# Optimization experiments

Hardware: AMD Instinct MI355X
Metric: run time of the kernel (lower is better)

## Reference

```python
import jax, jax.numpy as jnp
import numpy as np

# Static multi-scale feature pyramid shapes (value_shapes arg of MSDeformAttn.forward)
VALUE_SHAPES = ((80, 80), (40, 40), (20, 20), (10, 10))
N_HEADS, N_LEVELS, N_POINTS, D_MODEL = 8, 4, 4, 256


def setup_inputs() -> dict:
    key = jax.random.key(0)
    ks = jax.random.split(key, 11)
    bs, lq, d = 16, 1000, D_MODEL
    lv = sum(h * w for h, w in VALUE_SHAPES)  # 8500
    s = 0.02  # weight scale
    f32 = jnp.float32
    return {
        "query": jax.random.normal(ks[0], (bs, lq, d), f32),
        "refer_bbox": jax.random.uniform(ks[1], (bs, lq, 1, 4), f32),  # cxcywh in [0,1]
        "value": jax.random.normal(ks[2], (bs, lv, d), f32),
        "W_off": jax.random.normal(ks[3], (d, N_HEADS * N_LEVELS * N_POINTS * 2), f32) * s,
        "b_off": jax.random.normal(ks[4], (N_HEADS * N_LEVELS * N_POINTS * 2,), f32) * s,
        "W_attn": jax.random.normal(ks[5], (d, N_HEADS * N_LEVELS * N_POINTS), f32) * s,
        "b_attn": jax.random.normal(ks[6], (N_HEADS * N_LEVELS * N_POINTS,), f32) * s,
        "W_val": jax.random.normal(ks[7], (d, d), f32) * s,
        "b_val": jax.random.normal(ks[8], (d,), f32) * s,
        "W_out": jax.random.normal(ks[9], (d, d), f32) * s,
        "b_out": jax.random.normal(ks[10], (d,), f32) * s,
    }


def _bilinear_sample(v, x, y):
    """grid_sample(mode=bilinear, padding=zeros, align_corners=False) equivalent.
    v: [bs, H, W, nh, dh]; x, y: pixel-space coords [bs, lq, nh, P].
    Returns [bs, lq, nh, P, dh]."""
    bs, H, W, nh, dh = v.shape
    x0f = jnp.floor(x)
    y0f = jnp.floor(y)
    wx = x - x0f  # fractional weights
    wy = y - y0f
    x0 = x0f.astype(jnp.int32)
    y0 = y0f.astype(jnp.int32)
    x1, y1 = x0 + 1, y0 + 1
    b_idx = jnp.arange(bs)[:, None, None, None]
    h_idx = jnp.arange(nh)[None, None, :, None]

    def gather(yi, xi):
        valid = (xi >= 0) & (xi < W) & (yi >= 0) & (yi < H)
        xc = jnp.clip(xi, 0, W - 1)
        yc = jnp.clip(yi, 0, H - 1)
        val = v[b_idx, yc, xc, h_idx]  # [bs, lq, nh, P, dh]
        return val * valid[..., None].astype(v.dtype)

    return (gather(y0, x0) * ((1 - wx) * (1 - wy))[..., None]
            + gather(y0, x1) * (wx * (1 - wy))[..., None]
            + gather(y1, x0) * ((1 - wx) * wy)[..., None]
            + gather(y1, x1) * (wx * wy)[..., None])


def reference(query, refer_bbox, value, W_off, b_off, W_attn, b_attn, W_val, b_val, W_out, b_out):
    bs, lq, d = query.shape
    nh, L, P = N_HEADS, N_LEVELS, N_POINTS
    dh = d // nh

    # value projection
    v = value @ W_val + b_val  # [bs, lv, d]
    v = v.reshape(bs, -1, nh, dh)

    # sampling offsets and attention weights from query
    offsets = (query @ W_off + b_off).reshape(bs, lq, nh, L, P, 2)
    attn = (query @ W_attn + b_attn).reshape(bs, lq, nh, L * P)
    attn = jax.nn.softmax(attn, axis=-1).reshape(bs, lq, nh, L, P)

    # refer_bbox: [bs, lq, 1, 4] cxcywh; num_points == 4 branch
    add = offsets / P * refer_bbox[:, :, None, :, None, 2:] * 0.5
    loc = refer_bbox[:, :, None, :, None, :2] + add  # [bs, lq, nh, L, P, 2] in [0,1]

    out = jnp.zeros((bs, lq, nh, dh), query.dtype)
    start = 0
    for l, (H, W) in enumerate(VALUE_SHAPES):
        vl = v[:, start:start + H * W].reshape(bs, H, W, nh, dh)
        start += H * W
        ll = loc[:, :, :, l]  # [bs, lq, nh, P, 2]
        # normalized [0,1] -> pixel coords (align_corners=False): p = loc*size - 0.5
        x = ll[..., 0] * W - 0.5
        y = ll[..., 1] * H - 0.5
        sampled = _bilinear_sample(vl, x, y)  # [bs, lq, nh, P, dh]
        out = out + jnp.einsum('bqhpd,bqhp->bqhd', sampled, attn[:, :, :, l])

    out = out.reshape(bs, lq, d)
    return out @ W_out + b_out
```

## Files before the change

### kernel.cpp

```cpp
#include <hip/hip_runtime.h>
#include <cstdint>
#include <cstddef>


typedef unsigned short u16;
typedef u16 u16x8 __attribute__((ext_vector_type(8)));
typedef __bf16 bf16x8 __attribute__((ext_vector_type(8)));
typedef float f32x4 __attribute__((ext_vector_type(4)));

__device__ inline u16 f2bf(float f) {
  return __builtin_bit_cast(u16, (__bf16)f);
}

__device__ __forceinline__ void glds16(const void* g, void* l) {
  __builtin_amdgcn_global_load_lds(
      (const __attribute__((address_space(1))) void*)g,
      (__attribute__((address_space(3))) void*)l, 16, 0, 0);
}

__global__ __launch_bounds__(256) void wconv(
    const float* __restrict__ W0, const float* __restrict__ W1,
    const float* __restrict__ W2, const float* __restrict__ W3,
    u16* __restrict__ T0, u16* __restrict__ T1, u16* __restrict__ T2,
    u16* __restrict__ T3) {
  __shared__ u16 tile[64][65];
  const float* Ws[4] = {W0, W1, W2, W3};
  u16* Ts[4] = {T0, T1, T2, T3};
  const int Ns[4] = {256, 256, 128, 256};
  const int z = blockIdx.z;
  const int N = Ns[z];
  const int n0 = blockIdx.x * 64;
  if (n0 >= N) return;
  const int k0 = blockIdx.y * 64;
  const float* W = Ws[z];
  u16* Wt = Ts[z];
  const int tr = threadIdx.x >> 6;
  const int tc = threadIdx.x & 63;
#pragma unroll
  for (int r = 0; r < 64; r += 4)
    tile[r + tr][tc] = f2bf(W[(size_t)(k0 + r + tr) * N + n0 + tc]);
  __syncthreads();
#pragma unroll
  for (int r = 0; r < 64; r += 4)
    Wt[(size_t)(n0 + r + tr) * 256 + k0 + tc] = tile[tc][r + tr];
}

template <int WAVES, int NF, bool OUT_BF16>
__global__ __launch_bounds__(WAVES * 64, 1) void gemm_p2(
    const float* __restrict__ A, const u16* __restrict__ Wt,
    const float* __restrict__ bias, void* __restrict__ Cv,
    int M, int NT, int G) {
  constexpr int N = NF * 16;
  constexpr int TR = WAVES * 16;
  constexpr int STN = OUT_BF16 ? (NF / 2) : NF;
  __shared__ __align__(16) u16 Bls[N * 256];
  __shared__ __align__(16) float Asub[WAVES * 1024];
  const int wave = threadIdx.x >> 6;
  const int lane = threadIdx.x & 63;
  const int lr = lane & 15;
  const int lj = lane >> 4;

  constexpr int NI = NF * 8 / WAVES;
#pragma unroll
  for (int g = 0; g < NI; ++g) {
    int inst = wave * NI + g;
    int s2 = inst * 2 + (lane >> 5);
    int pc = lane & 31;
    int jc = pc ^ (s2 & 7);
    int c = (s2 & 15) * NF + (s2 >> 4);
    glds16((const char*)Wt + (size_t)c * 512 + (size_t)jc * 16,
           (char*)Bls + inst * 1024);
  }

  float bv[NF];
#pragma unroll
  for (int ni = 0; ni < NF; ++ni) bv[ni] = bias[lr * NF + ni];

  char* aw = (char*)Asub + wave * 4096;

  auto stageA = [&](int t, int s, int buf) {
#pragma unroll
    for (int i = 0; i < 2; ++i) {
      long row = (long)t * TR + wave * 16 + i * 8 + (lane >> 3);
      if (row > (long)M - 1) row = M - 1;
      int jc = (lane & 7) ^ (lane >> 3);
      glds16((const char*)A + row * 1024 + (size_t)s * 128 + (size_t)jc * 16,
             aw + buf * 2048 + i * 1024);
    }
  };

  stageA(blockIdx.x, 0, 0);
  stageA(blockIdx.x, 1, 1);
  __syncthreads();

  for (int t = blockIdx.x; t < NT; t += G) {
    f32x4 acc[NF] = {};
#pragma unroll
    for (int s = 0; s < 8; ++s) {
      if (s < 2) {
        if constexpr (STN == 8)
          asm volatile("s_waitcnt vmcnt(10)" ::: "memory");
        else
          asm volatile("s_waitcnt vmcnt(18)" ::: "memory");
      } else {
        asm volatile("s_waitcnt vmcnt(2)" ::: "memory");
      }
      const char* ab = aw + (s & 1) * 2048;
      const int sw = lr & 7;
      const int j0 = lj * 2;
      f32x4 a0 = *(const f32x4*)(ab + lr * 128 + ((j0 ^ sw) * 16));
      f32x4 a1 = *(const f32x4*)(ab + lr * 128 + (((j0 + 1) ^ sw) * 16));
      bf16x8 af;
      af[0] = (__bf16)a0[0]; af[1] = (__bf16)a0[1];
      af[2] = (__bf16)a0[2]; af[3] = (__bf16)a0[3];
      af[4] = (__bf16)a1[0]; af[5] = (__bf16)a1[1];
      af[6] = (__bf16)a1[2]; af[7] = (__bf16)a1[3];
#pragma unroll
      for (int ni = 0; ni < NF; ++ni) {
        int sl = ni * 16 + lr;
        int pc = (s * 4 + lj) ^ (sl & 7);
        bf16x8 b = __builtin_bit_cast(
            bf16x8, *(const u16x8*)((const char*)Bls + sl * 512 + pc * 16));
        acc[ni] = __builtin_amdgcn_mfma_f32_16x16x32_bf16(af, b, acc[ni],
                                                          0, 0, 0);
      }
      if (s < 6)
        stageA(t, s + 2, s & 1);
      else if (s == 6)
        stageA(t + G, 0, 0);
      else
        stageA(t + G, 1, 1);
    }
#pragma unroll
    for (int r = 0; r < 4; ++r) {
      long grow = (long)t * TR + wave * 16 + lj * 4 + r;
      if (grow >= M) continue;
      if (OUT_BF16) {
        bf16x8 lo, hi;
#pragma unroll
        for (int j = 0; j < 8; ++j) {
          lo[j] = (__bf16)(acc[j][r] + bv[j]);
          hi[j] = (__bf16)(acc[8 + j][r] + bv[8 + j]);
        }
        u16* pC = (u16*)Cv + grow * N + lr * NF;
        *(u16x8*)pC = __builtin_bit_cast(u16x8, lo);
        *(u16x8*)(pC + 8) = __builtin_bit_cast(u16x8, hi);
      } else {
#pragma unroll
        for (int q = 0; q < NF / 4; ++q) {
          f32x4 v;
#pragma unroll
          for (int j = 0; j < 4; ++j) v[j] = acc[q * 4 + j][r] + bv[q * 4 + j];
          *(f32x4*)((float*)Cv + grow * N + lr * NF + q * 4) = v;
        }
      }
    }
  }
}

__global__ __launch_bounds__(256, 4) void sample_fused(
    const float* __restrict__ Lgo, const float* __restrict__ Lga,
    const float* __restrict__ bbox, const u16* __restrict__ vbf,
    float* __restrict__ outs) {
  const int t = threadIdx.x;
  const int bi = blockIdx.x;
  const int xcd = bi & 7;
  const int j = bi >> 3;
  const int half = (j >= 125) ? 1 : 0;
  const int batch = xcd + 8 * half;
  const int qb = j - 125 * half;
  const int i0 = (batch * 125 + qb) * 8;

  __shared__ __align__(16) float sa[8 * 128];
  __shared__ __align__(16) int4 soff[1024];
  __shared__ __align__(16) float4 sw4[1024];
  __shared__ float sb[32];
  if (t < 32) sb[t] = bbox[(size_t)i0 * 4 + t];
  ((float4*)sa)[t] = ((const float4*)(Lga + (size_t)i0 * 128))[t];
  __syncthreads();
  if (t < 64) {
    int base = (t >> 3) * 128 + (t & 7) * 16;
    float mx = -3.0e38f;
#pragma unroll
    for (int k = 0; k < 16; ++k) mx = fmaxf(mx, sa[base + k]);
    float e[16];
    float s = 0.f;
#pragma unroll
    for (int k = 0; k < 16; ++k) {
      e[k] = __expf(sa[base + k] - mx);
      s += e[k];
    }
    float inv = 1.f / s;
#pragma unroll
    for (int k = 0; k < 16; ++k) sa[base + k] = e[k] * inv;
  }
  __syncthreads();
#pragma unroll
  for (int it = 0; it < 4; ++it) {
    int idx = it * 256 + t;
    int ql = idx >> 7;
    int rest = idx & 127;
    int h = rest >> 4;
    int pt = rest & 15;
    int l = pt >> 2;
    int W = 80 >> l;
    float2 off2 = *(const float2*)(Lgo + (size_t)(i0 + ql) * 256 + h * 32 + pt * 2);
    float xf = (sb[ql * 4 + 0] + off2.x * 0.125f * sb[ql * 4 + 2]) * (float)W - 0.5f;
    float yf = (sb[ql * 4 + 1] + off2.y * 0.125f * sb[ql * 4 + 3]) * (float)W - 0.5f;
    float aw = sa[ql * 128 + h * 16 + pt];
    float x0f = floorf(xf), y0f = floorf(yf);
    float wx = xf - x0f, wy = yf - y0f;
    int x0 = (int)x0f, y0 = (int)y0f;
    int x1 = x0 + 1, y1 = y0 + 1;
    float fx0 = (x0 >= 0 && x0 < W) ? 1.f : 0.f;
    float fx1 = (x1 >= 0 && x1 < W) ? 1.f : 0.f;
    float fy0 = (y0 >= 0 && y0 < W) ? 1.f : 0.f;
    float fy1 = (y1 >= 0 && y1 < W) ? 1.f : 0.f;
    int xc0 = min(max(x0, 0), W - 1), xc1 = min(max(x1, 0), W - 1);
    int yc0 = min(max(y0, 0), W - 1), yc1 = min(max(y1, 0), W - 1);
    int baseb = ((25600 - (25600 >> (2 * l))) / 3) * 512;
    int4 o;
    o.x = baseb + (yc0 * W + xc0) * 512;
    o.y = baseb + (yc0 * W + xc1) * 512;
    o.z = baseb + (yc1 * W + xc0) * 512;
    o.w = baseb + (yc1 * W + xc1) * 512;
    float aw0 = aw * (1.f - wy), aw1 = aw * wy;
    float4 wv;
    wv.x = aw0 * (1.f - wx) * fx0 * fy0;
    wv.y = aw0 * wx * fx1 * fy0;
    wv.z = aw1 * (1.f - wx) * fx0 * fy1;
    wv.w = aw1 * wx * fx1 * fy1;
    int phys = ql * 128 + h * 16 + (pt ^ h);
    soff[phys] = o;
    sw4[phys] = wv;
  }
  __syncthreads();
  const int ql = t >> 5;
  const int r = t & 31;
  const int h = r >> 2;
  const int cg = r & 3;
  const int chb = (h * 32 + cg * 8) * 2;
  const char* vbb = (const char*)vbf + (size_t)batch * 8500 * 512 + chb;
  float acc[8] = {};
#pragma unroll 2
  for (int pt = 0; pt < 16; ++pt) {
    int phys = ql * 128 + h * 16 + (pt ^ h);
    int4 o = soff[phys];
    float4 wv = sw4[phys];
    uint4 v00 = *(const uint4*)(vbb + o.x);
    uint4 v01 = *(const uint4*)(vbb + o.y);
    uint4 v10 = *(const uint4*)(vbb + o.z);
    uint4 v11 = *(const uint4*)(vbb + o.w);
    const uint32_t* p00 = (const uint32_t*)&v00;
    const uint32_t* p01 = (const uint32_t*)&v01;
    const uint32_t* p10 = (const uint32_t*)&v10;
    const uint32_t* p11 = (const uint32_t*)&v11;
#pragma unroll
    for (int k = 0; k < 4; ++k) {
      float a0 = __uint_as_float(p00[k] << 16);
      float a1 = __uint_as_float(p00[k] & 0xffff0000u);
      float b0 = __uint_as_float(p01[k] << 16);
      float b1 = __uint_as_float(p01[k] & 0xffff0000u);
      float c0 = __uint_as_float(p10[k] << 16);
      float c1 = __uint_as_float(p10[k] & 0xffff0000u);
      float d0 = __uint_as_float(p11[k] << 16);
      float d1 = __uint_as_float(p11[k] & 0xffff0000u);
      acc[2 * k] += wv.x * a0 + wv.y * b0 + wv.z * c0 + wv.w * d0;
      acc[2 * k + 1] += wv.x * a1 + wv.y * b1 + wv.z * c1 + wv.w * d1;
    }
  }
  float4* op = (float4*)(outs + (size_t)(i0 + ql) * 256 + h * 32 + cg * 8);
  op[0] = make_float4(acc[0], acc[1], acc[2], acc[3]);
  op[1] = make_float4(acc[4], acc[5], acc[6], acc[7]);
}

extern "C" void kernel_launch(void* const* d_in, const int* in_sizes, int n_in,
                              void* d_out, int out_size, void* d_ws, size_t ws_size,
                              hipStream_t stream) {
  const float* query  = (const float*)d_in[0];
  const float* bbox   = (const float*)d_in[1];
  const float* value  = (const float*)d_in[2];
  const float* W_off  = (const float*)d_in[3];
  const float* b_off  = (const float*)d_in[4];
  const float* W_attn = (const float*)d_in[5];
  const float* b_attn = (const float*)d_in[6];
  const float* W_val  = (const float*)d_in[7];
  const float* b_val  = (const float*)d_in[8];
  const float* W_out  = (const float*)d_in[9];
  const float* b_out  = (const float*)d_in[10];
  float* out = (float*)d_out;

  char* w = (char*)d_ws;
  u16* vbf     = (u16*)w;
  float* Lgo   = (float*)(w + 69632000);
  float* Lga   = (float*)(w + 86016000);
  float* outs  = (float*)(w + 94208000);
  u16* Wt_val  = (u16*)(w + 110592000);
  u16* Wt_off  = (u16*)(w + 110723072);
  u16* Wt_attn = (u16*)(w + 110854144);
  u16* Wt_out  = (u16*)(w + 110919680);

  const int M_v = 16 * 8500;
  const int M_q = 16 * 1000;

  wconv<<<dim3(4, 4, 4), 256, 0, stream>>>(W_val, W_off, W_attn, W_out,
                                           Wt_val, Wt_off, Wt_attn, Wt_out);
  gemm_p2<8, 16, true><<<256, 512, 0, stream>>>(
      value, Wt_val, b_val, (void*)vbf, M_v, 1063, 256);
  gemm_p2<4, 16, false><<<250, 256, 0, stream>>>(
      query, Wt_off, b_off, (void*)Lgo, M_q, 250, 250);
  gemm_p2<4, 8, false><<<250, 256, 0, stream>>>(
      query, Wt_attn, b_attn, (void*)Lga, M_q, 250, 250);
  sample_fused<<<2000, 256, 0, stream>>>(Lgo, Lga, bbox, vbf, outs);
  gemm_p2<4, 16, false><<<250, 256, 0, stream>>>(
      outs, Wt_out, b_out, (void*)out, M_q, 250, 250);
}
```

Before: 124.6 us.

## Split value projection GEMM into two column-half launches with wider blocks

The value projection GEMM now runs as two launches, each producing 128 of the 256 output columns. Each launch uses 16 waves per block and half the weight tile in LDS, and a new output-stride template parameter lets each half write into the shared bf16 value buffer. The vmcnt wait counts are adjusted for the smaller store count. The goal is more waves per CU and less LDS per block, at the cost of reading the fp32 value matrix twice and paying one extra launch.

```diff
diff --git a/kernel.cpp b/kernel.cpp
--- a/kernel.cpp
+++ b/kernel.cpp
@@ -45,14 +45,14 @@
     Wt[(size_t)(n0 + r + tr) * 256 + k0 + tc] = tile[tc][r + tr];
 }
 
-template <int WAVES, int NF, bool OUT_BF16>
+template <int WAVES, int NF, bool OUT_BF16, int CSTRIDE>
 __global__ __launch_bounds__(WAVES * 64, 1) void gemm_p2(
     const float* __restrict__ A, const u16* __restrict__ Wt,
     const float* __restrict__ bias, void* __restrict__ Cv,
     int M, int NT, int G) {
   constexpr int N = NF * 16;
   constexpr int TR = WAVES * 16;
-  constexpr int STN = OUT_BF16 ? (NF / 2) : NF;
+  constexpr int STN = OUT_BF16 ? (NF / 8) * 4 : NF;
   __shared__ __align__(16) u16 Bls[N * 256];
   __shared__ __align__(16) float Asub[WAVES * 1024];
   const int wave = threadIdx.x >> 6;
@@ -98,7 +98,9 @@
 #pragma unroll
     for (int s = 0; s < 8; ++s) {
       if (s < 2) {
-        if constexpr (STN == 8)
+        if constexpr (STN == 4)
+          asm volatile("s_waitcnt vmcnt(6)" ::: "memory");
+        else if constexpr (STN == 8)
           asm volatile("s_waitcnt vmcnt(10)" ::: "memory");
         else
           asm volatile("s_waitcnt vmcnt(18)" ::: "memory");
@@ -136,22 +138,22 @@
       long grow = (long)t * TR + wave * 16 + lj * 4 + r;
       if (grow >= M) continue;
       if (OUT_BF16) {
-        bf16x8 lo, hi;
-#pragma unroll
-        for (int j = 0; j < 8; ++j) {
-          lo[j] = (__bf16)(acc[j][r] + bv[j]);
-          hi[j] = (__bf16)(acc[8 + j][r] + bv[8 + j]);
+#pragma unroll
+        for (int q = 0; q < NF / 8; ++q) {
+          bf16x8 v8;
+#pragma unroll
+          for (int j = 0; j < 8; ++j)
+            v8[j] = (__bf16)(acc[q * 8 + j][r] + bv[q * 8 + j]);
+          u16* pC = (u16*)Cv + grow * CSTRIDE + lr * NF + q * 8;
+          *(u16x8*)pC = __builtin_bit_cast(u16x8, v8);
         }
-        u16* pC = (u16*)Cv + grow * N + lr * NF;
-        *(u16x8*)pC = __builtin_bit_cast(u16x8, lo);
-        *(u16x8*)(pC + 8) = __builtin_bit_cast(u16x8, hi);
       } else {
 #pragma unroll
         for (int q = 0; q < NF / 4; ++q) {
           f32x4 v;
 #pragma unroll
           for (int j = 0; j < 4; ++j) v[j] = acc[q * 4 + j][r] + bv[q * 4 + j];
-          *(f32x4*)((float*)Cv + grow * N + lr * NF + q * 4) = v;
+          *(f32x4*)((float*)Cv + grow * CSTRIDE + lr * NF + q * 4) = v;
         }
       }
     }
@@ -305,13 +307,16 @@
 
   wconv<<<dim3(4, 4, 4), 256, 0, stream>>>(W_val, W_off, W_attn, W_out,
                                            Wt_val, Wt_off, Wt_attn, Wt_out);
-  gemm_p2<8, 16, true><<<256, 512, 0, stream>>>(
-      value, Wt_val, b_val, (void*)vbf, M_v, 1063, 256);
-  gemm_p2<4, 16, false><<<250, 256, 0, stream>>>(
+  gemm_p2<16, 8, true, 256><<<256, 1024, 0, stream>>>(
+      value, Wt_val, b_val, (void*)vbf, M_v, 532, 256);
+  gemm_p2<16, 8, true, 256><<<256, 1024, 0, stream>>>(
+      value, Wt_val + 128 * 256, b_val + 128, (void*)(vbf + 128), M_v, 532,
+      256);
+  gemm_p2<4, 16, false, 256><<<250, 256, 0, stream>>>(
       query, Wt_off, b_off, (void*)Lgo, M_q, 250, 250);
-  gemm_p2<4, 8, false><<<250, 256, 0, stream>>>(
+  gemm_p2<4, 8, false, 128><<<250, 256, 0, stream>>>(
       query, Wt_attn, b_attn, (void*)Lga, M_q, 250, 250);
   sample_fused<<<2000, 256, 0, stream>>>(Lgo, Lga, bbox, vbf, outs);
-  gemm_p2<4, 16, false><<<250, 256, 0, stream>>>(
+  gemm_p2<4, 16, false, 256><<<250, 256, 0, stream>>>(
       outs, Wt_out, b_out, (void*)out, M_q, 250, 250);
 }
```

Result: slower. 147.3 us (+18.2%).
